# Optimization experiments

Hardware: AMD Instinct MI355X
Metric: run time of the kernel (lower is better)

Reference implementation:

```python
import jax, jax.numpy as jnp
import numpy as np

N = 12288
IN_F = 256
OUT_F = 128
ALPHA = 0.2  # LeakyReLU negative slope


def setup_inputs() -> dict:
    key = jax.random.key(0)
    k_x, k_adj, k_w, k_a1, k_a2 = jax.random.split(key, 5)
    x = jax.random.normal(k_x, (N, IN_F), dtype=jnp.float32)
    adj = jax.random.randint(k_adj, (N, N), 0, 2, dtype=jnp.int32)
    # Learned params (nn.Linear without bias). Kaiming-uniform-ish init scale.
    W = jax.random.normal(k_w, (IN_F, OUT_F), dtype=jnp.float32) / np.sqrt(IN_F)
    a1 = jax.random.normal(k_a1, (OUT_F,), dtype=jnp.float32) / np.sqrt(OUT_F)
    a2 = jax.random.normal(k_a2, (OUT_F,), dtype=jnp.float32) / np.sqrt(OUT_F)
    return {"x": x, "adj": adj, "W": W, "a1": a1, "a2": a2}


def reference(x, adj, W, a1, a2):
    # h = tran(x): [N, OUT_F]
    h = x @ W
    # e[i, j] = att1(h)[j] + att2(h)[i]  (unsqueeze(0) + unsqueeze(1))
    s1 = h @ a1  # [N]
    s2 = h @ a2  # [N]
    e = s1[None, :] + s2[:, None]            # [N, N]
    e = jnp.where(e > 0, e, ALPHA * e)       # LeakyReLU
    e = jnp.where(adj > 0, e, -jnp.inf)      # mask non-edges
    attn = jax.nn.softmax(e, axis=1)         # row softmax (dropout=0 / eval)
    return attn @ h                          # [N, OUT_F]
```

## Files before the change

kernel.cpp:

```cpp
#include <hip/hip_runtime.h>
#include <hip/hip_bf16.h>
#include <hip/hip_fp16.h>

constexpr int NR = 12288;
constexpr int KF = 256;
constexpr int DF = 128;
constexpr int CH = 16;
constexpr int CW = NR / CH;
constexpr int NSTEP = CW / 32;
constexpr int ROWS = 256;
constexpr int BMW = NR / 32;
#define NEGBIG (-1e30f)

typedef __attribute__((ext_vector_type(8))) __bf16 bf16x8;
typedef __attribute__((ext_vector_type(4))) float  f32x4;

__device__ __forceinline__ unsigned short f2bf(float f) {
    union { float f; unsigned u; } v; v.f = f;
    unsigned r = v.u + 0x7FFFu + ((v.u >> 16) & 1u);
    return (unsigned short)(r >> 16);
}

__device__ __forceinline__ void gload16(const void* g, void* l) {
    __builtin_amdgcn_global_load_lds(
        (const __attribute__((address_space(1))) void*)g,
        (__attribute__((address_space(3))) void*)l, 16, 0, 0);
}

__device__ __forceinline__ unsigned fmap(float f) {
    unsigned b = __float_as_uint(f);
    return (b & 0x80000000u) ? ~b : (b | 0x80000000u);
}
__device__ __forceinline__ float funmap(unsigned m) {
    unsigned b = (m & 0x80000000u) ? (m ^ 0x80000000u) : ~m;
    return __uint_as_float(b);
}

__global__ __launch_bounds__(256) void k_compress(
    const int* __restrict__ adj, unsigned* __restrict__ bm, unsigned* __restrict__ gmxu)
{
    if (blockIdx.x == 0 && threadIdx.x == 0) gmxu[0] = 0u;
    const int lane = threadIdx.x & 63;
    const unsigned sh = (lane & 7) * 4;
    size_t i = (size_t)blockIdx.x * 256 + threadIdx.x;
    const size_t total4 = (size_t)NR * NR / 4;
    const size_t stride = (size_t)gridDim.x * 256;
    const int4* a4 = (const int4*)adj;
    for (; i < total4; i += stride) {
        int4 a = a4[i];
        unsigned nib = (unsigned)(a.x > 0) | ((unsigned)(a.y > 0) << 1)
                     | ((unsigned)(a.z > 0) << 2) | ((unsigned)(a.w > 0) << 3);
        unsigned v = nib << sh;
        v |= __shfl_xor(v, 1);
        v |= __shfl_xor(v, 2);
        v |= __shfl_xor(v, 4);
        if ((lane & 7) == 0) bm[i >> 3] = v;
    }
}

__global__ __launch_bounds__(256) void k_gemm_h(
    const float* __restrict__ x, const float* __restrict__ W,
    const float* __restrict__ a1, const float* __restrict__ a2,
    unsigned short* __restrict__ hbT, float* __restrict__ s1, float* __restrict__ s2,
    unsigned* __restrict__ gmxu)
{
    __shared__ __align__(16) float xs[64][65];
    __shared__ __align__(16) float ws[64][132];
    const int t  = threadIdx.x;
    const int tx = t & 15, ty = t >> 4;
    const int lane = t & 63;
    const int rowbase = blockIdx.x * 64;

    float acc[4][8];
#pragma unroll
    for (int i = 0; i < 4; ++i)
#pragma unroll
        for (int j = 0; j < 8; ++j) acc[i][j] = 0.f;

    for (int kt = 0; kt < KF; kt += 64) {
        {
            int row = t >> 2, k0 = (t & 3) * 16;
            const float4* src = (const float4*)(x + (size_t)(rowbase + row) * KF + kt + k0);
            float4 v0 = src[0], v1 = src[1], v2 = src[2], v3 = src[3];
            xs[row][k0+ 0]=v0.x; xs[row][k0+ 1]=v0.y; xs[row][k0+ 2]=v0.z; xs[row][k0+ 3]=v0.w;
            xs[row][k0+ 4]=v1.x; xs[row][k0+ 5]=v1.y; xs[row][k0+ 6]=v1.z; xs[row][k0+ 7]=v1.w;
            xs[row][k0+ 8]=v2.x; xs[row][k0+ 9]=v2.y; xs[row][k0+10]=v2.z; xs[row][k0+11]=v2.w;
            xs[row][k0+12]=v3.x; xs[row][k0+13]=v3.y; xs[row][k0+14]=v3.z; xs[row][k0+15]=v3.w;
        }
        {
            int k = t >> 2, c0 = (t & 3) * 32;
            const float4* src = (const float4*)(W + (size_t)(kt + k) * DF + c0);
#pragma unroll
            for (int j = 0; j < 8; ++j)
                *(float4*)&ws[k][c0 + j * 4] = src[j];
        }
        __syncthreads();
#pragma unroll 4
        for (int k = 0; k < 64; ++k) {
            float xv[4];
#pragma unroll
            for (int ri = 0; ri < 4; ++ri) xv[ri] = xs[ty * 4 + ri][k];
            float4 w0 = *(float4*)&ws[k][tx * 8];
            float4 w1 = *(float4*)&ws[k][tx * 8 + 4];
#pragma unroll
            for (int ri = 0; ri < 4; ++ri) {
                acc[ri][0] += xv[ri] * w0.x; acc[ri][1] += xv[ri] * w0.y;
                acc[ri][2] += xv[ri] * w0.z; acc[ri][3] += xv[ri] * w0.w;
                acc[ri][4] += xv[ri] * w1.x; acc[ri][5] += xv[ri] * w1.y;
                acc[ri][6] += xv[ri] * w1.z; acc[ri][7] += xv[ri] * w1.w;
            }
        }
        __syncthreads();
    }
#pragma unroll
    for (int ci = 0; ci < 8; ++ci) {
        int col = tx * 8 + ci;
        ushort4 u;
        u.x = f2bf(acc[0][ci]); u.y = f2bf(acc[1][ci]);
        u.z = f2bf(acc[2][ci]); u.w = f2bf(acc[3][ci]);
        *(ushort4*)(hbT + (size_t)col * NR + rowbase + ty * 4) = u;
    }
    float4 a1lo = *(const float4*)(a1 + tx * 8), a1hi = *(const float4*)(a1 + tx * 8 + 4);
    float4 a2lo = *(const float4*)(a2 + tx * 8), a2hi = *(const float4*)(a2 + tx * 8 + 4);
    float lmax = NEGBIG;
#pragma unroll
    for (int ri = 0; ri < 4; ++ri) {
        float p1 = acc[ri][0]*a1lo.x + acc[ri][1]*a1lo.y + acc[ri][2]*a1lo.z + acc[ri][3]*a1lo.w
                 + acc[ri][4]*a1hi.x + acc[ri][5]*a1hi.y + acc[ri][6]*a1hi.z + acc[ri][7]*a1hi.w;
        float p2 = acc[ri][0]*a2lo.x + acc[ri][1]*a2lo.y + acc[ri][2]*a2lo.z + acc[ri][3]*a2lo.w
                 + acc[ri][4]*a2hi.x + acc[ri][5]*a2hi.y + acc[ri][6]*a2hi.z + acc[ri][7]*a2hi.w;
#pragma unroll
        for (int off = 8; off > 0; off >>= 1) {
            p1 += __shfl_xor(p1, off);
            p2 += __shfl_xor(p2, off);
        }
        if (tx == 0) {
            s1[rowbase + ty * 4 + ri] = p1;
            s2[rowbase + ty * 4 + ri] = p2;
        }
        lmax = fmaxf(lmax, p1);
    }
    lmax = fmaxf(lmax, __shfl_xor(lmax, 16));
    lmax = fmaxf(lmax, __shfl_xor(lmax, 32));
    if (lane == 0) atomicMax(gmxu, fmap(lmax));
}

__global__ __launch_bounds__(1024, 4) void k_flash(
    const unsigned* __restrict__ bm, const unsigned short* __restrict__ hbT,
    const float* __restrict__ s1, const float* __restrict__ s2,
    const unsigned* __restrict__ gmxu,
    __half* __restrict__ num, float* __restrict__ lC)
{
    __shared__ __align__(16) unsigned short hbtring[3][4096];
    __shared__ __align__(16) unsigned       bmlds[ROWS][28];
    __shared__ __align__(16) float          s1lds[CW];

    const int t    = threadIdx.x;
    const int wid  = t >> 6, lane = t & 63;
    const int r    = lane & 15, g = lane >> 4;
    const int rowb = blockIdx.x * ROWS;
    const int prow = rowb + wid * 16 + r;
    const int chunk = blockIdx.y;
    const int j0 = chunk * CW;

    if (t < CW / 4) *(float4*)&s1lds[t * 4] = *(const float4*)(s1 + j0 + t * 4);
#pragma unroll
    for (int i = 0; i < 2; ++i) {
        int idx = i * 1024 + t;
        if (idx < 1536) {
            int brow = idx / 6, bk = idx % 6;
            uint4 w = *(const uint4*)(bm + (size_t)(rowb + brow) * BMW + chunk * NSTEP + bk * 4);
            *(uint4*)&bmlds[brow][bk * 4] = w;
        }
    }

    const float gm  = funmap(gmxu[0]);
    const float s2r = s2[prow];
    const float zub = s2r + gm;
    const float Mi  = fmaxf(zub, 0.2f * zub);

    const int hrow  = wid * 16 + (lane >> 2);
    const int hcol8 = ((lane & 3) ^ ((lane >> 3) & 3)) * 8;
    const unsigned short* hgp0 = hbT + (size_t)hrow * NR + j0 + hcol8;
    const int hldso0 = wid * 16 * 64;
    const int h_base = r * 64 + ((g ^ ((r >> 1) & 3)) * 16);

#define ISSUE(st) do { \
        const int sl_ = (st) % 3; \
        const size_t go_ = (size_t)(((st) % NSTEP) * 32); \
        if (wid < 8) gload16(hgp0 + go_, (char*)&hbtring[sl_][0] + hldso0); \
    } while (0)

    float lsum = 0.f;
    f32x4 acc[8];
#pragma unroll
    for (int f = 0; f < 8; ++f) acc[f] = f32x4{0.f, 0.f, 0.f, 0.f};

    ISSUE(0);
    ISSUE(1);

    const unsigned* bmrow = &bmlds[wid * 16 + r][0];
    const unsigned gsh = g * 8;

    for (int j = 0; j < NSTEP; ++j) {
        if (wid < 8) asm volatile("s_waitcnt vmcnt(1) lgkmcnt(0)" ::: "memory");
        else         asm volatile("s_waitcnt lgkmcnt(0)" ::: "memory");
        __builtin_amdgcn_s_barrier();
        __builtin_amdgcn_sched_barrier(0);
        ISSUE(j + 2);

        const unsigned mw = bmrow[j] >> gsh;
        const float4 Sa = *(const float4*)&s1lds[j * 32 + g * 8];
        const float4 Sb = *(const float4*)&s1lds[j * 32 + g * 8 + 4];

        bf16x8 pf;
#define PROC(bi, ss, idx) { \
            float t0 = (ss) + s2r; \
            float lr = fmaxf(t0, 0.2f * t0); \
            float q  = __expf(lr - Mi); \
            float p  = ((mw >> (bi)) & 1u) ? q : 0.f; \
            lsum += p; \
            pf[idx] = (__bf16)p; }
        PROC(0, Sa.x, 0) PROC(1, Sa.y, 1)
        PROC(2, Sa.z, 2) PROC(3, Sa.w, 3)
        PROC(4, Sb.x, 4) PROC(5, Sb.y, 5)
        PROC(6, Sb.z, 6) PROC(7, Sb.w, 7)
#undef PROC

        const int sl = j % 3;
        const char* hb = (const char*)&hbtring[sl][0] + h_base;
#pragma unroll
        for (int f = 0; f < 8; ++f) {
            bf16x8 bfr = *(const bf16x8*)(hb + f * 1024);
            acc[f] = __builtin_amdgcn_mfma_f32_16x16x32_bf16(pf, bfr, acc[f], 0, 0, 0);
        }
    }
#undef ISSUE

    lsum += __shfl_xor(lsum, 16);
    lsum += __shfl_xor(lsum, 32);
    if (g == 0) lC[(size_t)chunk * NR + prow] = lsum;

    __half* nb = num + (size_t)chunk * NR * DF;
#pragma unroll
    for (int f = 0; f < 8; ++f)
#pragma unroll
        for (int q = 0; q < 4; ++q) {
            int row = rowb + wid * 16 + g * 4 + q;
            nb[(size_t)row * DF + f * 16 + r] = __float2half(acc[f][q]);
        }
}

__global__ __launch_bounds__(256) void k_comb(
    const __half* __restrict__ num, const float* __restrict__ lC,
    float* __restrict__ out)
{
    const int t   = threadIdx.x;
    const int row = blockIdx.x * 2 + (t >> 7);
    const int f   = t & 127;
    float L = 0.f, o = 0.f;
    for (int c = 0; c < CH; ++c) {
        L += lC[(size_t)c * NR + row];
        o += __half2float(num[(size_t)c * NR * DF + (size_t)row * DF + f]);
    }
    out[(size_t)row * DF + f] = o / L;
}

extern "C" void kernel_launch(void* const* d_in, const int* in_sizes, int n_in,
                              void* d_out, int out_size, void* d_ws, size_t ws_size,
                              hipStream_t stream)
{
    const float* x   = (const float*)d_in[0];
    const int*   adj = (const int*)d_in[1];
    const float* W   = (const float*)d_in[2];
    const float* a1  = (const float*)d_in[3];
    const float* a2  = (const float*)d_in[4];
    float* out = (float*)d_out;

    char* p = (char*)d_ws;
    unsigned short* hbT = (unsigned short*)p; p += (size_t)DF * NR * 2;
    unsigned*       bmw = (unsigned*)p;       p += (size_t)NR * BMW * 4;
    float*          s1  = (float*)p;          p += (size_t)NR * 4;
    float*          s2  = (float*)p;          p += (size_t)NR * 4;
    unsigned*       gmxu = (unsigned*)p;      p += 256;
    __half*         numb = (__half*)p;        p += (size_t)CH * NR * DF * 2;
    float*          lC   = (float*)p;

    k_compress<<<2048, 256, 0, stream>>>(adj, bmw, gmxu);
    k_gemm_h<<<NR / 64, 256, 0, stream>>>(x, W, a1, a2, hbT, s1, s2, gmxu);
    k_flash<<<dim3(NR / ROWS, CH), 1024, 0, stream>>>(bmw, hbT, s1, s2, gmxu, numb, lC);
    k_comb<<<NR / 2, 256, 0, stream>>>(numb, lC, out);
}
```

Baseline: 249.3 us.

## Halve flash block to 8 waves, each computing two 16-row tiles sharing B fragments

Each wave now processes two 16-row groups (rows r and r+128) of the 256-row block, so the block shrinks from 16 to 8 waves. Every B fragment read from shared memory now feeds two MFMAs, which halves LDS traffic per MFMA and removes the idle non-loading waves. The cost is doubled accumulator registers per thread (64 fp32 acc) and half as many waves per block to hide latency.

```diff
diff --git a/kernel.cpp b/kernel.cpp
--- a/kernel.cpp
+++ b/kernel.cpp
@@ -145,7 +145,7 @@
     if (lane == 0) atomicMax(gmxu, fmap(lmax));
 }
 
-__global__ __launch_bounds__(1024, 4) void k_flash(
+__global__ __launch_bounds__(512, 4) void k_flash(
     const unsigned* __restrict__ bm, const unsigned short* __restrict__ hbT,
     const float* __restrict__ s1, const float* __restrict__ s2,
     const unsigned* __restrict__ gmxu,
@@ -159,25 +159,26 @@
     const int wid  = t >> 6, lane = t & 63;
     const int r    = lane & 15, g = lane >> 4;
     const int rowb = blockIdx.x * ROWS;
-    const int prow = rowb + wid * 16 + r;
+    const int prowA = rowb + wid * 16 + r;
+    const int prowB = prowA + 128;
     const int chunk = blockIdx.y;
     const int j0 = chunk * CW;
 
     if (t < CW / 4) *(float4*)&s1lds[t * 4] = *(const float4*)(s1 + j0 + t * 4);
 #pragma unroll
-    for (int i = 0; i < 2; ++i) {
-        int idx = i * 1024 + t;
-        if (idx < 1536) {
-            int brow = idx / 6, bk = idx % 6;
-            uint4 w = *(const uint4*)(bm + (size_t)(rowb + brow) * BMW + chunk * NSTEP + bk * 4);
-            *(uint4*)&bmlds[brow][bk * 4] = w;
-        }
-    }
-
-    const float gm  = funmap(gmxu[0]);
-    const float s2r = s2[prow];
-    const float zub = s2r + gm;
-    const float Mi  = fmaxf(zub, 0.2f * zub);
+    for (int i = 0; i < 3; ++i) {
+        int idx = i * 512 + t;
+        int brow = idx / 6, bk = idx % 6;
+        uint4 w = *(const uint4*)(bm + (size_t)(rowb + brow) * BMW + chunk * NSTEP + bk * 4);
+        *(uint4*)&bmlds[brow][bk * 4] = w;
+    }
+
+    const float gm   = funmap(gmxu[0]);
+    const float s2rA = s2[prowA];
+    const float s2rB = s2[prowB];
+    const float zubA = s2rA + gm, zubB = s2rB + gm;
+    const float MiA  = fmaxf(zubA, 0.2f * zubA);
+    const float MiB  = fmaxf(zubB, 0.2f * zubB);
 
     const int hrow  = wid * 16 + (lane >> 2);
     const int hcol8 = ((lane & 3) ^ ((lane >> 3) & 3)) * 8;
@@ -188,43 +189,51 @@
 #define ISSUE(st) do { \
         const int sl_ = (st) % 3; \
         const size_t go_ = (size_t)(((st) % NSTEP) * 32); \
-        if (wid < 8) gload16(hgp0 + go_, (char*)&hbtring[sl_][0] + hldso0); \
+        gload16(hgp0 + go_, (char*)&hbtring[sl_][0] + hldso0); \
     } while (0)
 
-    float lsum = 0.f;
-    f32x4 acc[8];
-#pragma unroll
-    for (int f = 0; f < 8; ++f) acc[f] = f32x4{0.f, 0.f, 0.f, 0.f};
+    float lsumA = 0.f, lsumB = 0.f;
+    f32x4 accA[8], accB[8];
+#pragma unroll
+    for (int f = 0; f < 8; ++f) {
+        accA[f] = f32x4{0.f, 0.f, 0.f, 0.f};
+        accB[f] = f32x4{0.f, 0.f, 0.f, 0.f};
+    }
 
     ISSUE(0);
     ISSUE(1);
 
-    const unsigned* bmrow = &bmlds[wid * 16 + r][0];
+    const unsigned* bmrowA = &bmlds[wid * 16 + r][0];
+    const unsigned* bmrowB = &bmlds[128 + wid * 16 + r][0];
     const unsigned gsh = g * 8;
 
     for (int j = 0; j < NSTEP; ++j) {
-        if (wid < 8) asm volatile("s_waitcnt vmcnt(1) lgkmcnt(0)" ::: "memory");
-        else         asm volatile("s_waitcnt lgkmcnt(0)" ::: "memory");
+        asm volatile("s_waitcnt vmcnt(1) lgkmcnt(0)" ::: "memory");
         __builtin_amdgcn_s_barrier();
         __builtin_amdgcn_sched_barrier(0);
         ISSUE(j + 2);
 
-        const unsigned mw = bmrow[j] >> gsh;
+        const unsigned mwA = bmrowA[j] >> gsh;
+        const unsigned mwB = bmrowB[j] >> gsh;
         const float4 Sa = *(const float4*)&s1lds[j * 32 + g * 8];
         const float4 Sb = *(const float4*)&s1lds[j * 32 + g * 8 + 4];
 
-        bf16x8 pf;
-#define PROC(bi, ss, idx) { \
-            float t0 = (ss) + s2r; \
+        bf16x8 pfA, pfB;
+#define PROC(mw_, s2r_, Mi_, lsum_, pf_, bi, ss, idx) { \
+            float t0 = (ss) + (s2r_); \
             float lr = fmaxf(t0, 0.2f * t0); \
-            float q  = __expf(lr - Mi); \
-            float p  = ((mw >> (bi)) & 1u) ? q : 0.f; \
-            lsum += p; \
-            pf[idx] = (__bf16)p; }
-        PROC(0, Sa.x, 0) PROC(1, Sa.y, 1)
-        PROC(2, Sa.z, 2) PROC(3, Sa.w, 3)
-        PROC(4, Sb.x, 4) PROC(5, Sb.y, 5)
-        PROC(6, Sb.z, 6) PROC(7, Sb.w, 7)
+            float q  = __expf(lr - (Mi_)); \
+            float p  = (((mw_) >> (bi)) & 1u) ? q : 0.f; \
+            lsum_ += p; \
+            pf_[idx] = (__bf16)p; }
+        PROC(mwA, s2rA, MiA, lsumA, pfA, 0, Sa.x, 0) PROC(mwA, s2rA, MiA, lsumA, pfA, 1, Sa.y, 1)
+        PROC(mwA, s2rA, MiA, lsumA, pfA, 2, Sa.z, 2) PROC(mwA, s2rA, MiA, lsumA, pfA, 3, Sa.w, 3)
+        PROC(mwA, s2rA, MiA, lsumA, pfA, 4, Sb.x, 4) PROC(mwA, s2rA, MiA, lsumA, pfA, 5, Sb.y, 5)
+        PROC(mwA, s2rA, MiA, lsumA, pfA, 6, Sb.z, 6) PROC(mwA, s2rA, MiA, lsumA, pfA, 7, Sb.w, 7)
+        PROC(mwB, s2rB, MiB, lsumB, pfB, 0, Sa.x, 0) PROC(mwB, s2rB, MiB, lsumB, pfB, 1, Sa.y, 1)
+        PROC(mwB, s2rB, MiB, lsumB, pfB, 2, Sa.z, 2) PROC(mwB, s2rB, MiB, lsumB, pfB, 3, Sa.w, 3)
+        PROC(mwB, s2rB, MiB, lsumB, pfB, 4, Sb.x, 4) PROC(mwB, s2rB, MiB, lsumB, pfB, 5, Sb.y, 5)
+        PROC(mwB, s2rB, MiB, lsumB, pfB, 6, Sb.z, 6) PROC(mwB, s2rB, MiB, lsumB, pfB, 7, Sb.w, 7)
 #undef PROC
 
         const int sl = j % 3;
@@ -232,22 +241,29 @@
 #pragma unroll
         for (int f = 0; f < 8; ++f) {
             bf16x8 bfr = *(const bf16x8*)(hb + f * 1024);
-            acc[f] = __builtin_amdgcn_mfma_f32_16x16x32_bf16(pf, bfr, acc[f], 0, 0, 0);
+            accA[f] = __builtin_amdgcn_mfma_f32_16x16x32_bf16(pfA, bfr, accA[f], 0, 0, 0);
+            accB[f] = __builtin_amdgcn_mfma_f32_16x16x32_bf16(pfB, bfr, accB[f], 0, 0, 0);
         }
     }
 #undef ISSUE
 
-    lsum += __shfl_xor(lsum, 16);
-    lsum += __shfl_xor(lsum, 32);
-    if (g == 0) lC[(size_t)chunk * NR + prow] = lsum;
+    lsumA += __shfl_xor(lsumA, 16);
+    lsumA += __shfl_xor(lsumA, 32);
+    lsumB += __shfl_xor(lsumB, 16);
+    lsumB += __shfl_xor(lsumB, 32);
+    if (g == 0) {
+        lC[(size_t)chunk * NR + prowA] = lsumA;
+        lC[(size_t)chunk * NR + prowB] = lsumB;
+    }
 
     __half* nb = num + (size_t)chunk * NR * DF;
 #pragma unroll
     for (int f = 0; f < 8; ++f)
 #pragma unroll
         for (int q = 0; q < 4; ++q) {
-            int row = rowb + wid * 16 + g * 4 + q;
-            nb[(size_t)row * DF + f * 16 + r] = __float2half(acc[f][q]);
+            int rowA = rowb + wid * 16 + g * 4 + q;
+            nb[(size_t)rowA * DF + f * 16 + r]         = __float2half(accA[f][q]);
+            nb[(size_t)(rowA + 128) * DF + f * 16 + r] = __float2half(accB[f][q]);
         }
 }
 
@@ -288,6 +304,6 @@
 
     k_compress<<<2048, 256, 0, stream>>>(adj, bmw, gmxu);
     k_gemm_h<<<NR / 64, 256, 0, stream>>>(x, W, a1, a2, hbT, s1, s2, gmxu);
-    k_flash<<<dim3(NR / ROWS, CH), 1024, 0, stream>>>(bmw, hbT, s1, s2, gmxu, numb, lC);
+    k_flash<<<dim3(NR / ROWS, CH), 512, 0, stream>>>(bmw, hbT, s1, s2, gmxu, numb, lC);
     k_comb<<<NR / 2, 256, 0, stream>>>(numb, lC, out);
 }
```

Measured after the change: 233.4 us. 6.4% less time.
